# Kernel tuning notes

Measured on AMD Instinct MI355X. Metric: run time of the kernel, lower is better.

Reference implementation:

```python
import jax, jax.numpy as jnp
import numpy as np


def setup_inputs() -> dict:
    key = jax.random.key(0)
    k1, k2, k3, k4 = jax.random.split(key, 4)
    B, C, H, W = 8, 64, 64, 64
    K = C // 8
    x = jax.random.normal(k1, (B, C, H, W), dtype=jnp.float32)
    # 1x1 conv weights (no bias): stored as [out_ch, in_ch]
    Wf = jax.random.normal(k2, (K, C), dtype=jnp.float32) * 0.05
    Wg = jax.random.normal(k3, (K, C), dtype=jnp.float32) * 0.05
    Wh = jax.random.normal(k4, (C, C), dtype=jnp.float32) * 0.05
    # gamma initialized to zero in the module; use a nonzero value so the
    # attention path contributes to the output (and gradients) in testing.
    gamma = jnp.array([0.5], dtype=jnp.float32)
    return {"x": x, "Wf": Wf, "Wg": Wg, "Wh": Wh, "gamma": gamma}


def reference(x, Wf, Wg, Wh, gamma):
    B, C, H, W = x.shape
    N = H * W
    xf = x.reshape(B, C, N)                       # [B, C, N]
    f = jnp.einsum('kc,bcn->bkn', Wf, xf)         # [B, C//8, N]
    g = jnp.einsum('kc,bcn->bkn', Wg, xf)         # [B, C//8, N]
    h = jnp.einsum('oc,bcn->bon', Wh, xf)         # [B, C, N]
    # beta[b, i, j] = f[b,:,i] . g[b,:,j]  (unscaled attention logits)
    beta = jnp.einsum('bki,bkj->bij', f, g)       # [B, N, N]
    beta = jax.nn.softmax(beta, axis=-1)
    # res[b, c, i] = sum_j h[b, c, j] * beta[b, i, j]
    res = jnp.einsum('bcj,bij->bci', h, beta)     # [B, C, N]
    res = res.reshape(B, C, H, W)
    return gamma * res + x
```

## Files before the change

kernel.cpp:

```cpp
#include <hip/hip_runtime.h>

typedef float f32x4 __attribute__((ext_vector_type(4)));
typedef float f32x16 __attribute__((ext_vector_type(16)));
typedef short s16x8 __attribute__((ext_vector_type(8)));
typedef short s16x4 __attribute__((ext_vector_type(4)));
typedef unsigned short u16;

#define NB 8
#define NC 64
#define NN 4096
#define NK 8

__device__ __forceinline__ u16 f2bf_rne(float f) {
    unsigned u = __float_as_uint(f);
    u += 0x7FFFu + ((u >> 16) & 1u);
    return (u16)(u >> 16);
}
__device__ __forceinline__ float bf2f(u16 v) {
    return __uint_as_float(((unsigned)v) << 16);
}
__device__ __forceinline__ unsigned cvt_pk_bf16(float lo, float hi) {
    unsigned r;
    asm("v_cvt_pk_bf16_f32 %0, %1, %2" : "=v"(r) : "v"(lo), "v"(hi));
    return r;
}
__device__ __forceinline__ void pl32_swap(unsigned &a, unsigned &b) {
    asm("v_permlane32_swap_b32 %0, %1" : "+v"(a), "+v"(b));
}

#define Z16 ((f32x16){0.f,0.f,0.f,0.f,0.f,0.f,0.f,0.f,0.f,0.f,0.f,0.f,0.f,0.f,0.f,0.f})

__global__ __launch_bounds__(256, 4)
void precompute_qgh(const float* __restrict__ x,
                    const float* __restrict__ Wf,
                    const float* __restrict__ Wg,
                    const float* __restrict__ Wh,
                    u16* __restrict__ Qw, u16* __restrict__ Gw,
                    u16* __restrict__ Hw)
{
    const int b  = blockIdx.y;
    const int n0 = blockIdx.x * 64;
    const int t  = threadIdx.x;
    const int wave = t >> 6, lane = t & 63, col = lane & 15, quad = lane >> 4;
    const float* xb = x + (size_t)b * NC * NN;

    __shared__ __align__(16) u16 WL[80][72];
    __shared__ __align__(16) u16 XT[64][72];

    #pragma unroll
    for (int r5 = 0; r5 < 5; r5++) {
        int v = r5 * 256 + t;
        int m = v >> 4, ks = (v & 15) << 2;
        const float* src = (m < 64) ? (Wh + m * 64 + ks)
                         : (m < 72) ? (Wf + (m - 64) * 64 + ks)
                                    : (Wg + (m - 72) * 64 + ks);
        f32x4 wv = *(const f32x4*)src;
        *(unsigned*)&WL[m][ks]     = (unsigned)f2bf_rne(wv[0]) | ((unsigned)f2bf_rne(wv[1]) << 16);
        *(unsigned*)&WL[m][ks + 2] = (unsigned)f2bf_rne(wv[2]) | ((unsigned)f2bf_rne(wv[3]) << 16);
    }
    #pragma unroll
    for (int r4 = 0; r4 < 4; r4++) {
        int v = r4 * 256 + t;
        int c = v >> 4, ns = (v & 15) << 2;
        f32x4 xv = *(const f32x4*)(xb + (size_t)c * NN + n0 + ns);
        #pragma unroll
        for (int e = 0; e < 4; e++) XT[ns + e][c] = f2bf_rne(xv[e]);
    }
    __syncthreads();

    const int n = n0 + wave * 16 + col;
    s16x8 bfrag[2], afrag[5][2];
    #pragma unroll
    for (int s = 0; s < 2; s++)
        bfrag[s] = *(const s16x8*)&XT[wave * 16 + col][s * 32 + quad * 8];
    #pragma unroll
    for (int mt = 0; mt < 5; mt++)
        #pragma unroll
        for (int s = 0; s < 2; s++)
            afrag[mt][s] = *(const s16x8*)&WL[mt * 16 + col][s * 32 + quad * 8];

    f32x4 d[5];
    #pragma unroll
    for (int mt = 0; mt < 5; mt++) d[mt] = (f32x4){0.f, 0.f, 0.f, 0.f};
    #pragma unroll
    for (int s = 0; s < 2; s++)
        #pragma unroll
        for (int mt = 0; mt < 5; mt++)
            d[mt] = __builtin_amdgcn_mfma_f32_16x16x32_bf16(afrag[mt][s], bfrag[s], d[mt], 0, 0, 0);

    u16* Hb = Hw + (size_t)b * NC * NN;
    #pragma unroll
    for (int mt = 0; mt < 4; mt++)
        #pragma unroll
        for (int r = 0; r < 4; r++)
            Hb[(size_t)(mt * 16 + quad * 4 + r) * NN + n] = f2bf_rne(d[mt][r]);
    #pragma unroll
    for (int r = 0; r < 4; r++) {
        int m = quad * 4 + r;
        u16 v = f2bf_rne(d[4][r]);
        if (m < 8) Qw[((size_t)b * NN + n) * NK + m]       = v;
        else       Gw[((size_t)b * NN + n) * NK + (m - 8)] = v;
    }
}

__global__ __launch_bounds__(256, 4)
void attention_fa(const u16* __restrict__ Qw, const u16* __restrict__ Gw,
                  const u16* __restrict__ Hw,
                  u16* __restrict__ Opart, float* __restrict__ Lpart,
                  int jspan)
{
    const int b    = blockIdx.y;
    const int i0   = blockIdx.x * 128;
    const int part = blockIdx.z;
    const int t    = threadIdx.x;
    const int wave = t >> 6, lane = t & 63, col = lane & 31, hi = lane >> 5;

    __shared__ __align__(16) u16 Vl[2][64][64];

    const u16* Qb = Qw + (size_t)b * NN * NK;
    const u16* Gb = Gw + (size_t)b * NN * NK;
    const u16* Hb = Hw + (size_t)b * NC * NN;

    s16x8 qf;
    #pragma unroll
    for (int q = 0; q < 8; q++) ((u16*)&qf)[q] = 0;
    if (hi == 0) qf = *(const s16x8*)(Qb + (size_t)(i0 + wave * 32 + col) * NK);

    s16x8 ones;
    #pragma unroll
    for (int q = 0; q < 8; q++) ((u16*)&ones)[q] = 0x3F80;

    f32x16 oacc[2];
    oacc[0] = Z16; oacc[1] = Z16;
    f32x16 lacc = Z16;

    const int jbase  = part * jspan;
    const int chunks = jspan / 64;
    const int vc = t >> 3, vseg = t & 7;
    const int swsl = (vseg ^ (vc & 7)) * 8;
    const int c7x8 = (col & 7) * 8;

    s16x8 vreg0 = *(const s16x8*)(Hb + (size_t)vc * NN + jbase + swsl);
    s16x8 vreg1 = *(const s16x8*)(Hb + (size_t)(32 + vc) * NN + jbase + swsl);

    for (int cc = 0; cc < chunks; cc++) {
        const int j0 = jbase + cc * 64;
        u16* vb = &Vl[cc & 1][0][0];

        s16x8 ga0, ga1;
        #pragma unroll
        for (int q = 0; q < 8; q++) { ((u16*)&ga0)[q] = 0; ((u16*)&ga1)[q] = 0; }
        if (hi == 0) {
            ga0 = *(const s16x8*)(Gb + (size_t)(j0 + col) * NK);
            ga1 = *(const s16x8*)(Gb + (size_t)(j0 + 32 + col) * NK);
        }

        *(s16x8*)(vb + vc * 64 + vseg * 8)        = vreg0;
        *(s16x8*)(vb + (32 + vc) * 64 + vseg * 8) = vreg1;
        vreg0 = *(const s16x8*)(Hb + (size_t)vc * NN + j0 + 64 + swsl);
        vreg1 = *(const s16x8*)(Hb + (size_t)(32 + vc) * NN + j0 + 64 + swsl);

        __syncthreads();

        #pragma unroll
        for (int jt = 0; jt < 2; jt++) {
            f32x16 S = __builtin_amdgcn_mfma_f32_32x32x16_bf16(jt ? ga1 : ga0, qf, Z16, 0, 0, 0);
            #pragma unroll
            for (int r = 0; r < 16; r++) S[r] = __expf(S[r]);
            #pragma unroll
            for (int s2 = 0; s2 < 2; s2++) {
                unsigned w0 = cvt_pk_bf16(S[8*s2+0], S[8*s2+1]);
                unsigned w2 = cvt_pk_bf16(S[8*s2+4], S[8*s2+5]);
                unsigned w1 = cvt_pk_bf16(S[8*s2+2], S[8*s2+3]);
                unsigned w3 = cvt_pk_bf16(S[8*s2+6], S[8*s2+7]);
                pl32_swap(w0, w2);
                pl32_swap(w1, w3);
                union { s16x8 v; unsigned u[4]; } pb;
                pb.u[0] = w0; pb.u[1] = w1; pb.u[2] = w2; pb.u[3] = w3;
                lacc = __builtin_amdgcn_mfma_f32_32x32x16_bf16(ones, pb.v, lacc, 0, 0, 0);
                const int soff = ((jt * 4 + s2 * 2 + hi) * 8) ^ c7x8;
                s16x8 va0 = *(const s16x8*)(vb + col * 64 + soff);
                s16x8 va1 = *(const s16x8*)(vb + (32 + col) * 64 + soff);
                oacc[0] = __builtin_amdgcn_mfma_f32_32x32x16_bf16(va0, pb.v, oacc[0], 0, 0, 0);
                oacc[1] = __builtin_amdgcn_mfma_f32_32x32x16_bf16(va1, pb.v, oacc[1], 0, 0, 0);
            }
        }
    }

    if (hi == 0)
        Lpart[((size_t)part * NB + b) * NN + i0 + wave * 32 + col] = lacc[0];

    __syncthreads();
    u16* OT = &Vl[0][0][0];
    #pragma unroll
    for (int ct = 0; ct < 2; ct++)
        #pragma unroll
        for (int r = 0; r < 16; r++) {
            int c = ct * 32 + (r & 3) + 8 * (r >> 2) + 4 * hi;
            OT[c * 128 + wave * 32 + col] = f2bf_rne(oacc[ct][r]);
        }
    __syncthreads();
    u16* Ob = Opart + ((size_t)part * NB + b) * NC * NN;
    const int oc = t >> 2, oq = t & 3;
    #pragma unroll
    for (int e = 0; e < 4; e++)
        *(s16x8*)(Ob + (size_t)oc * NN + i0 + oq * 32 + e * 8) =
            *(const s16x8*)(OT + oc * 128 + oq * 32 + e * 8);
}

__global__ __launch_bounds__(256, 4)
void reduce_out(const u16* __restrict__ Opart, const float* __restrict__ Lpart,
                const float* __restrict__ x, const float* __restrict__ gamma,
                float* __restrict__ out, int parts)
{
    const int tid  = blockIdx.x * 256 + threadIdx.x;
    const int base = tid * 4;
    const int bc   = base >> 12;
    const int b    = bc >> 6;
    const int ii   = base & (NN - 1);

    float s[4] = {0.f, 0.f, 0.f, 0.f};
    f32x4 l4 = (f32x4){0.f, 0.f, 0.f, 0.f};
    for (int p = 0; p < parts; p++) {
        s16x4 ov = *(const s16x4*)(Opart + ((size_t)p * NB * NC + bc) * NN + ii);
        l4 += *(const f32x4*)(Lpart + ((size_t)p * NB + b) * NN + ii);
        #pragma unroll
        for (int e = 0; e < 4; e++) s[e] += bf2f((u16)ov[e]);
    }
    const float g = gamma[0];
    const f32x4 xv = *(const f32x4*)(x + base);
    f32x4 o;
    #pragma unroll
    for (int e = 0; e < 4; e++) o[e] = g * (s[e] / l4[e]) + xv[e];
    *(f32x4*)(out + base) = o;
}

extern "C" void kernel_launch(void* const* d_in, const int* in_sizes, int n_in,
                              void* d_out, int out_size, void* d_ws, size_t ws_size,
                              hipStream_t stream) {
    const float* x     = (const float*)d_in[0];
    const float* Wf    = (const float*)d_in[1];
    const float* Wg    = (const float*)d_in[2];
    const float* Wh    = (const float*)d_in[3];
    const float* gamma = (const float*)d_in[4];
    float* out = (float*)d_out;

    u16* Qw = (u16*)d_ws;
    u16* Gw = Qw + (size_t)NB * NN * NK;
    u16* Hw = Gw + (size_t)NB * NN * NK;
    u16* Opart = Hw + (size_t)NB * NC * NN;

    const size_t fixed = (size_t)(2 * NB * NN * NK + NB * NC * NN) * 2;
    int parts = 4;
    while (parts > 1) {
        size_t need = fixed + (size_t)parts * NB * NC * NN * 2
                            + (size_t)parts * NB * NN * 4 + 8192;
        if (need <= ws_size) break;
        parts >>= 1;
    }
    float* Lpart = (float*)(Opart + (size_t)parts * NB * NC * NN);
    const int jspan = NN / parts;

    precompute_qgh<<<dim3(64, NB), 256, 0, stream>>>(x, Wf, Wg, Wh, Qw, Gw, Hw);
    attention_fa<<<dim3(32, NB, parts), 256, 0, stream>>>(Qw, Gw, Hw, Opart, Lpart, jspan);
    reduce_out<<<dim3((NB * NC * NN) / 1024), 256, 0, stream>>>(Opart, Lpart, x, gamma, out, parts);
}
```

Baseline: 111.0 us.

## Fuse split-K reduction into attention kernel with intra-block wave pairs

Removes the separate reduce_out kernel and the Opart/Lpart global round trip. Each block now handles 64 query rows and splits the key range into two halves across wave pairs, combining the partial output and softmax denominator in shared memory before writing gamma*res + x directly. It also folds log2(e) into Wf so the inner loop can use the hardware exp2 instead of __expf. The grid becomes 512 blocks, each streaming half the key range, and launch bounds drop to 2 blocks per SM, which may reduce occupancy and latency hiding.

```diff
diff --git a/kernel.cpp b/kernel.cpp
--- a/kernel.cpp
+++ b/kernel.cpp
@@ -26,6 +26,9 @@
 }
 __device__ __forceinline__ void pl32_swap(unsigned &a, unsigned &b) {
     asm("v_permlane32_swap_b32 %0, %1" : "+v"(a), "+v"(b));
+}
+__device__ __forceinline__ float exp2_hw(float x) {
+    return __builtin_amdgcn_exp2f(x);
 }
 
 #define Z16 ((f32x16){0.f,0.f,0.f,0.f,0.f,0.f,0.f,0.f,0.f,0.f,0.f,0.f,0.f,0.f,0.f,0.f})
@@ -54,9 +57,10 @@
         const float* src = (m < 64) ? (Wh + m * 64 + ks)
                          : (m < 72) ? (Wf + (m - 64) * 64 + ks)
                                     : (Wg + (m - 72) * 64 + ks);
+        const float scl = (m >= 64 && m < 72) ? 1.44269504088896f : 1.0f;
         f32x4 wv = *(const f32x4*)src;
-        *(unsigned*)&WL[m][ks]     = (unsigned)f2bf_rne(wv[0]) | ((unsigned)f2bf_rne(wv[1]) << 16);
-        *(unsigned*)&WL[m][ks + 2] = (unsigned)f2bf_rne(wv[2]) | ((unsigned)f2bf_rne(wv[3]) << 16);
+        *(unsigned*)&WL[m][ks]     = (unsigned)f2bf_rne(wv[0] * scl) | ((unsigned)f2bf_rne(wv[1] * scl) << 16);
+        *(unsigned*)&WL[m][ks + 2] = (unsigned)f2bf_rne(wv[2] * scl) | ((unsigned)f2bf_rne(wv[3] * scl) << 16);
     }
     #pragma unroll
     for (int r4 = 0; r4 < 4; r4++) {
@@ -103,19 +107,19 @@
     }
 }
 
-__global__ __launch_bounds__(256, 4)
-void attention_fa(const u16* __restrict__ Qw, const u16* __restrict__ Gw,
-                  const u16* __restrict__ Hw,
-                  u16* __restrict__ Opart, float* __restrict__ Lpart,
-                  int jspan)
+__global__ __launch_bounds__(256, 2)
+void attention_fused(const u16* __restrict__ Qw, const u16* __restrict__ Gw,
+                     const u16* __restrict__ Hw,
+                     const float* __restrict__ x, const float* __restrict__ gamma,
+                     float* __restrict__ out)
 {
-    const int b    = blockIdx.y;
-    const int i0   = blockIdx.x * 128;
-    const int part = blockIdx.z;
-    const int t    = threadIdx.x;
+    const int b  = blockIdx.y;
+    const int i0 = blockIdx.x * 64;
+    const int t  = threadIdx.x;
     const int wave = t >> 6, lane = t & 63, col = lane & 31, hi = lane >> 5;
-
-    __shared__ __align__(16) u16 Vl[2][64][64];
+    const int p = wave >> 1, wi = wave & 1;
+
+    __shared__ __align__(16) u16 Vl[2][2][64][64];
 
     const u16* Qb = Qw + (size_t)b * NN * NK;
     const u16* Gb = Gw + (size_t)b * NN * NK;
@@ -124,7 +128,7 @@
     s16x8 qf;
     #pragma unroll
     for (int q = 0; q < 8; q++) ((u16*)&qf)[q] = 0;
-    if (hi == 0) qf = *(const s16x8*)(Qb + (size_t)(i0 + wave * 32 + col) * NK);
+    if (hi == 0) qf = *(const s16x8*)(Qb + (size_t)(i0 + wi * 32 + col) * NK);
 
     s16x8 ones;
     #pragma unroll
@@ -134,18 +138,20 @@
     oacc[0] = Z16; oacc[1] = Z16;
     f32x16 lacc = Z16;
 
-    const int jbase  = part * jspan;
-    const int chunks = jspan / 64;
-    const int vc = t >> 3, vseg = t & 7;
+    const int jbase = p * 2048;
+    const int tp = t & 127;
+    const int vc = tp >> 3, vseg = tp & 7;
     const int swsl = (vseg ^ (vc & 7)) * 8;
     const int c7x8 = (col & 7) * 8;
 
-    s16x8 vreg0 = *(const s16x8*)(Hb + (size_t)vc * NN + jbase + swsl);
-    s16x8 vreg1 = *(const s16x8*)(Hb + (size_t)(32 + vc) * NN + jbase + swsl);
-
-    for (int cc = 0; cc < chunks; cc++) {
+    s16x8 vreg[4];
+    #pragma unroll
+    for (int u = 0; u < 4; u++)
+        vreg[u] = *(const s16x8*)(Hb + (size_t)(vc + 16 * u) * NN + jbase + swsl);
+
+    for (int cc = 0; cc < 32; cc++) {
         const int j0 = jbase + cc * 64;
-        u16* vb = &Vl[cc & 1][0][0];
+        u16* vb = &Vl[p][cc & 1][0][0];
 
         s16x8 ga0, ga1;
         #pragma unroll
@@ -155,10 +161,12 @@
             ga1 = *(const s16x8*)(Gb + (size_t)(j0 + 32 + col) * NK);
         }
 
-        *(s16x8*)(vb + vc * 64 + vseg * 8)        = vreg0;
-        *(s16x8*)(vb + (32 + vc) * 64 + vseg * 8) = vreg1;
-        vreg0 = *(const s16x8*)(Hb + (size_t)vc * NN + j0 + 64 + swsl);
-        vreg1 = *(const s16x8*)(Hb + (size_t)(32 + vc) * NN + j0 + 64 + swsl);
+        #pragma unroll
+        for (int u = 0; u < 4; u++)
+            *(s16x8*)(vb + (vc + 16 * u) * 64 + vseg * 8) = vreg[u];
+        #pragma unroll
+        for (int u = 0; u < 4; u++)
+            vreg[u] = *(const s16x8*)(Hb + (size_t)(vc + 16 * u) * NN + j0 + 64 + swsl);
 
         __syncthreads();
 
@@ -166,7 +174,7 @@
         for (int jt = 0; jt < 2; jt++) {
             f32x16 S = __builtin_amdgcn_mfma_f32_32x32x16_bf16(jt ? ga1 : ga0, qf, Z16, 0, 0, 0);
             #pragma unroll
-            for (int r = 0; r < 16; r++) S[r] = __expf(S[r]);
+            for (int r = 0; r < 16; r++) S[r] = exp2_hw(S[r]);
             #pragma unroll
             for (int s2 = 0; s2 < 2; s2++) {
                 unsigned w0 = cvt_pk_bf16(S[8*s2+0], S[8*s2+1]);
@@ -187,52 +195,54 @@
         }
     }
 
-    if (hi == 0)
-        Lpart[((size_t)part * NB + b) * NN + i0 + wave * 32 + col] = lacc[0];
-
-    __syncthreads();
-    u16* OT = &Vl[0][0][0];
-    #pragma unroll
-    for (int ct = 0; ct < 2; ct++)
-        #pragma unroll
-        for (int r = 0; r < 16; r++) {
-            int c = ct * 32 + (r & 3) + 8 * (r >> 2) + 4 * hi;
-            OT[c * 128 + wave * 32 + col] = f2bf_rne(oacc[ct][r]);
+    float* Of = (float*)&Vl[0][0][0][0];
+    float* Lf = Of + 2 * 64 * 32;
+    u16*  OT  = (u16*)(Lf + 64);
+    const float g = gamma[0];
+
+    __syncthreads();
+    if (p == 1) {
+        #pragma unroll
+        for (int ct = 0; ct < 2; ct++)
+            #pragma unroll
+            for (int r = 0; r < 16; r++) {
+                int c = ct * 32 + (r & 3) + 8 * (r >> 2) + 4 * hi;
+                Of[(wi * 64 + c) * 32 + col] = oacc[ct][r];
+            }
+        if (hi == 0) Lf[wi * 32 + col] = lacc[0];
+    }
+    __syncthreads();
+    if (p == 0) {
+        const float scale = g / (lacc[0] + Lf[wi * 32 + col]);
+        const int i = wi * 32 + col;
+        #pragma unroll
+        for (int ct = 0; ct < 2; ct++)
+            #pragma unroll
+            for (int r = 0; r < 16; r++) {
+                int c = ct * 32 + (r & 3) + 8 * (r >> 2) + 4 * hi;
+                float o = (oacc[ct][r] + Of[(wi * 64 + c) * 32 + col]) * scale;
+                OT[c * 64 + (((i >> 3) ^ (c & 7)) << 3) + (i & 7)] = f2bf_rne(o);
+            }
+    }
+    __syncthreads();
+
+    const int oc = t >> 2, q4 = t & 3;
+    s16x8 v0 = *(const s16x8*)&OT[oc * 64 + (((2 * q4)     ^ (oc & 7)) << 3)];
+    s16x8 v1 = *(const s16x8*)&OT[oc * 64 + (((2 * q4 + 1) ^ (oc & 7)) << 3)];
+    const float* xr = x   + ((size_t)b * NC + oc) * NN + i0 + q4 * 16;
+    float*      orow = out + ((size_t)b * NC + oc) * NN + i0 + q4 * 16;
+    #pragma unroll
+    for (int e = 0; e < 4; e++) {
+        f32x4 xv = *(const f32x4*)(xr + e * 4);
+        f32x4 ov;
+        #pragma unroll
+        for (int k = 0; k < 4; k++) {
+            u16 val = (e < 2) ? (u16)((u16*)&v0)[e * 4 + k]
+                              : (u16)((u16*)&v1)[(e - 2) * 4 + k];
+            ov[k] = bf2f(val) + xv[k];
         }
-    __syncthreads();
-    u16* Ob = Opart + ((size_t)part * NB + b) * NC * NN;
-    const int oc = t >> 2, oq = t & 3;
-    #pragma unroll
-    for (int e = 0; e < 4; e++)
-        *(s16x8*)(Ob + (size_t)oc * NN + i0 + oq * 32 + e * 8) =
-            *(const s16x8*)(OT + oc * 128 + oq * 32 + e * 8);
-}
-
-__global__ __launch_bounds__(256, 4)
-void reduce_out(const u16* __restrict__ Opart, const float* __restrict__ Lpart,
-                const float* __restrict__ x, const float* __restrict__ gamma,
-                float* __restrict__ out, int parts)
-{
-    const int tid  = blockIdx.x * 256 + threadIdx.x;
-    const int base = tid * 4;
-    const int bc   = base >> 12;
-    const int b    = bc >> 6;
-    const int ii   = base & (NN - 1);
-
-    float s[4] = {0.f, 0.f, 0.f, 0.f};
-    f32x4 l4 = (f32x4){0.f, 0.f, 0.f, 0.f};
-    for (int p = 0; p < parts; p++) {
-        s16x4 ov = *(const s16x4*)(Opart + ((size_t)p * NB * NC + bc) * NN + ii);
-        l4 += *(const f32x4*)(Lpart + ((size_t)p * NB + b) * NN + ii);
-        #pragma unroll
-        for (int e = 0; e < 4; e++) s[e] += bf2f((u16)ov[e]);
-    }
-    const float g = gamma[0];
-    const f32x4 xv = *(const f32x4*)(x + base);
-    f32x4 o;
-    #pragma unroll
-    for (int e = 0; e < 4; e++) o[e] = g * (s[e] / l4[e]) + xv[e];
-    *(f32x4*)(out + base) = o;
+        *(f32x4*)(orow + e * 4) = ov;
+    }
 }
 
 extern "C" void kernel_launch(void* const* d_in, const int* in_sizes, int n_in,
@@ -248,20 +258,7 @@
     u16* Qw = (u16*)d_ws;
     u16* Gw = Qw + (size_t)NB * NN * NK;
     u16* Hw = Gw + (size_t)NB * NN * NK;
-    u16* Opart = Hw + (size_t)NB * NC * NN;
-
-    const size_t fixed = (size_t)(2 * NB * NN * NK + NB * NC * NN) * 2;
-    int parts = 4;
-    while (parts > 1) {
-        size_t need = fixed + (size_t)parts * NB * NC * NN * 2
-                            + (size_t)parts * NB * NN * 4 + 8192;
-        if (need <= ws_size) break;
-        parts >>= 1;
-    }
-    float* Lpart = (float*)(Opart + (size_t)parts * NB * NC * NN);
-    const int jspan = NN / parts;
 
     precompute_qgh<<<dim3(64, NB), 256, 0, stream>>>(x, Wf, Wg, Wh, Qw, Gw, Hw);
-    attention_fa<<<dim3(32, NB, parts), 256, 0, stream>>>(Qw, Gw, Hw, Opart, Lpart, jspan);
-    reduce_out<<<dim3((NB * NC * NN) / 1024), 256, 0, stream>>>(Opart, Lpart, x, gamma, out, parts);
-}
+    attention_fused<<<dim3(64, NB), 256, 0, stream>>>(Qw, Gw, Hw, x, gamma, out);
+}
```

After: 105.2 us. 1.05x faster.
